# Kernel tuning notes

Measured on AMD Instinct MI355X. Metric: run time of the kernel, lower is better.

## Reference

```python
import jax, jax.numpy as jnp
import numpy as np

LOOPS = 2
NUM_GROUPS = 4
EXPERTS_PER_GROUP = 2
NUM_EXPERTS = NUM_GROUPS * EXPERTS_PER_GROUP
GROUPS_TOP_K = 2
TOP_K = 1
RMS_EPS = 1e-6
EPS = 1e-9


def setup_inputs() -> dict:
    key = jax.random.key(0)
    ks = jax.random.split(key, 6)
    B, S, D, F = 2, 1024, 1024, 2048
    return {
        "z": jax.random.normal(ks[0], (B, S, D), jnp.float32),
        "norm_w": jnp.ones((D,), jnp.float32),
        "w_macro": jax.random.normal(ks[1], (NUM_GROUPS, D), jnp.float32) * (D ** -0.5),
        "w_micro": jax.random.normal(ks[2], (NUM_GROUPS, EXPERTS_PER_GROUP, D), jnp.float32) * (D ** -0.5),
        "w1": jax.random.normal(ks[3], (NUM_EXPERTS, F, D), jnp.float32) * (D ** -0.5),
        "w2": jax.random.normal(ks[4], (NUM_EXPERTS, D, F), jnp.float32) * (F ** -0.5),
    }


def _rmsnorm(x, w):
    return x * jax.lax.rsqrt(jnp.mean(x * x, axis=-1, keepdims=True) + RMS_EPS) * w


def _combine_weights(x_flat, w_macro, w_micro):
    """Dense [T, E] combine matrix equivalent to the sort-based dispatch."""
    T = x_flat.shape[0]
    macro = jax.nn.softmax(x_flat @ w_macro.T, axis=-1)                    # [T, G]
    mvals, midx = jax.lax.top_k(macro, GROUPS_TOP_K)                       # [T, Gk]
    mvals = mvals / (jnp.sum(mvals, axis=-1, keepdims=True) + EPS)
    micro = jax.nn.softmax(jnp.einsum('td,ged->tge', x_flat, w_micro), axis=-1)  # [T, G, Eg]
    uvals, uidx = jax.lax.top_k(micro, TOP_K)                              # [T, G, k]
    uvals = uvals / (jnp.sum(uvals, axis=-1, keepdims=True) + EPS)
    tok = jnp.arange(T)
    combine = jnp.zeros((T, NUM_EXPERTS), x_flat.dtype)
    for s in range(GROUPS_TOP_K):
        g = midx[:, s]                                                     # [T]
        wg = mvals[:, s:s + 1]                                             # [T, 1]
        li = uidx[tok, g]                                                  # [T, k] local expert ids in group g
        lv = uvals[tok, g]                                                 # [T, k]
        eidx = g[:, None] * EXPERTS_PER_GROUP + li                         # [T, k] global expert ids
        combine = combine.at[tok[:, None], eidx].add(lv * wg)
    return combine


def reference(z, norm_w, w_macro, w_micro, w1, w2):
    B, S, D = z.shape
    T = B * S
    for _ in range(LOOPS):
        zn = _rmsnorm(z, norm_w)
        x = zn.reshape(T, D)
        combine = _combine_weights(x, w_macro, w_micro)                    # [T, E]
        # Dense equivalent of gather -> per-expert FFN -> weighted index_add
        h = jax.nn.silu(jnp.einsum('td,efd->tef', x, w1))                  # [T, E, F]
        y = jnp.einsum('tef,edf->ted', h, w2)                              # [T, E, D]
        mixed = jnp.einsum('ted,te->td', y, combine)                       # [T, D]
        z = z + mixed.reshape(B, S, D)
    return z
```

## Files before the change

### kernel.cpp

```cpp
#include <hip/hip_runtime.h>
#include <cstdint>
#include <cstddef>

#define T_TOK 2048
#define DDIM  1024
#define FDIM  2048

typedef __attribute__((ext_vector_type(8))) short bf16x8;
typedef __attribute__((ext_vector_type(4))) float f32x4;

static __device__ __forceinline__ float b2f(unsigned short u) {
  union { unsigned int i; float f; } v; v.i = ((unsigned int)u) << 16; return v.f;
}
static __device__ __forceinline__ unsigned short f2b(float f) {
  unsigned int x = __float_as_uint(f);
  return (unsigned short)((x + 0x7fffu + ((x >> 16) & 1u)) >> 16);
}
static __device__ __forceinline__ unsigned int pack2(float a, float b) {
  return (unsigned int)f2b(a) | ((unsigned int)f2b(b) << 16);
}

__global__ void k_probe(const unsigned int* __restrict__ nw, int* __restrict__ flag) {
  if (threadIdx.x == 0) flag[0] = (nw[0] == 0x3F800000u) ? 0 : 1;
}

__global__ void k_init(const void* __restrict__ zin, float* __restrict__ z32,
                       const int* __restrict__ flag) {
  const int i = blockIdx.x * blockDim.x + threadIdx.x;
  float4 f;
  if (flag[0]) {
    ushort4 u = ((const ushort4*)zin)[i];
    f.x = b2f(u.x); f.y = b2f(u.y); f.z = b2f(u.z); f.w = b2f(u.w);
  } else {
    f = ((const float4*)zin)[i];
  }
  ((float4*)z32)[i] = f;
}

__global__ void k_out(const float* __restrict__ z32, void* __restrict__ out,
                      const int* __restrict__ flag) {
  const int i = blockIdx.x * blockDim.x + threadIdx.x;
  const float4 a = ((const float4*)z32)[i];
  if (flag[0]) {
    ushort4 o; o.x = f2b(a.x); o.y = f2b(a.y); o.z = f2b(a.z); o.w = f2b(a.w);
    ((ushort4*)out)[i] = o;
  } else {
    ((float4*)out)[i] = a;
  }
}

__global__ void k_rms_route(const float* __restrict__ z32,
                            const void* __restrict__ nw,
                            const void* __restrict__ wmac,
                            const void* __restrict__ wmic,
                            const int* __restrict__ flag,
                            unsigned short* __restrict__ xh,
                            unsigned short* __restrict__ xl,
                            float* __restrict__ logits,
                            const int base)
{
  const int tl = blockIdx.x;
  const int t  = base + tl;
  const int tid = threadIdx.x;
  const int lane = tid & 63, wv = tid >> 6;
  const int isbf = flag[0];
  const float4 zv = ((const float4*)(z32 + (size_t)t * DDIM))[tid];
  float ss = zv.x*zv.x + zv.y*zv.y + zv.z*zv.z + zv.w*zv.w;
  #pragma unroll
  for (int o = 32; o > 0; o >>= 1) ss += __shfl_down(ss, o);
  __shared__ float red[4];
  __shared__ float lred[12][4];
  if (lane == 0) red[wv] = ss;
  __syncthreads();
  const float tot = red[0] + red[1] + red[2] + red[3];
  const float scale = 1.f / sqrtf(tot * (1.f / DDIM) + 1e-6f);
  float4 nwv;
  if (isbf) {
    ushort4 u = ((const ushort4*)nw)[tid];
    nwv.x = b2f(u.x); nwv.y = b2f(u.y); nwv.z = b2f(u.z); nwv.w = b2f(u.w);
  } else {
    nwv = ((const float4*)nw)[tid];
  }
  float4 xn;
  xn.x = zv.x * scale * nwv.x;
  xn.y = zv.y * scale * nwv.y;
  xn.z = zv.z * scale * nwv.z;
  xn.w = zv.w * scale * nwv.w;
  ushort4 h4, l4;
  h4.x = f2b(xn.x); l4.x = f2b(xn.x - b2f(h4.x));
  h4.y = f2b(xn.y); l4.y = f2b(xn.y - b2f(h4.y));
  h4.z = f2b(xn.z); l4.z = f2b(xn.z - b2f(h4.z));
  h4.w = f2b(xn.w); l4.w = f2b(xn.w - b2f(h4.w));
  ((ushort4*)(xh + (size_t)tl * DDIM))[tid] = h4;
  ((ushort4*)(xl + (size_t)tl * DDIM))[tid] = l4;

  float part[12];
  #pragma unroll
  for (int r = 0; r < 4; r++) {
    float4 w;
    if (isbf) {
      ushort4 u = ((const ushort4*)wmac)[r * 256 + tid];
      w.x = b2f(u.x); w.y = b2f(u.y); w.z = b2f(u.z); w.w = b2f(u.w);
    } else {
      w = ((const float4*)wmac)[r * 256 + tid];
    }
    part[r] = xn.x*w.x + xn.y*w.y + xn.z*w.z + xn.w*w.w;
  }
  #pragma unroll
  for (int r = 0; r < 8; r++) {
    float4 w;
    if (isbf) {
      ushort4 u = ((const ushort4*)wmic)[r * 256 + tid];
      w.x = b2f(u.x); w.y = b2f(u.y); w.z = b2f(u.z); w.w = b2f(u.w);
    } else {
      w = ((const float4*)wmic)[r * 256 + tid];
    }
    part[4 + r] = xn.x*w.x + xn.y*w.y + xn.z*w.z + xn.w*w.w;
  }
  #pragma unroll
  for (int r = 0; r < 12; r++) {
    float v = part[r];
    #pragma unroll
    for (int o = 32; o > 0; o >>= 1) v += __shfl_down(v, o);
    if (lane == 0) lred[r][wv] = v;
  }
  __syncthreads();
  if (tid < 12)
    logits[tl * 12 + tid] = lred[tid][0] + lred[tid][1] + lred[tid][2] + lred[tid][3];
}

__global__ void k_route_a(const float* __restrict__ logits, int* __restrict__ eidx,
                          float* __restrict__ cw, int* __restrict__ counts, const int Tc)
{
  const int t = blockIdx.x * 256 + threadIdx.x;
  if (t >= Tc) return;
  const float* lg = logits + t * 12;
  float p[4];
  float m = fmaxf(fmaxf(lg[0], lg[1]), fmaxf(lg[2], lg[3]));
  float s = 0.f;
  #pragma unroll
  for (int i = 0; i < 4; i++) { p[i] = expf(lg[i] - m); s += p[i]; }
  #pragma unroll
  for (int i = 0; i < 4; i++) p[i] /= s;
  int i1 = 0;
  #pragma unroll
  for (int i = 1; i < 4; i++) if (p[i] > p[i1]) i1 = i;
  int i2 = (i1 == 0) ? 1 : 0;
  #pragma unroll
  for (int i = 0; i < 4; i++) if (i != i1 && p[i] > p[i2]) i2 = i;
  const float denom = p[i1] + p[i2] + 1e-9f;
  const int gs[2] = { i1, i2 };
  #pragma unroll
  for (int sI = 0; sI < 2; sI++) {
    const int g = gs[sI];
    const float wg = p[g] / denom;
    const float u0 = lg[4 + 2*g], u1 = lg[4 + 2*g + 1];
    const int li = (u1 > u0) ? 1 : 0;
    const float uval = 1.f / (1.f + expf(-fabsf(u0 - u1)));
    const float lv = uval / (uval + 1e-9f);
    const int e = g * 2 + li;
    eidx[t*2 + sI] = e;
    cw[t*2 + sI] = wg * lv;
    atomicAdd(&counts[e], 1);
  }
}

__global__ void k_route_b(const int* __restrict__ counts, int* __restrict__ offsets) {
  if (threadIdx.x == 0) {
    int o = 0;
    for (int e = 0; e < 8; e++) { offsets[e] = o; o += counts[e]; }
    offsets[8] = o;
  }
}

__global__ void k_route_c(const int* __restrict__ eidx, const float* __restrict__ cw,
                          const int* __restrict__ offsets, int* __restrict__ counts2,
                          int* __restrict__ tok, float* __restrict__ wof, const int Tc)
{
  const int t = blockIdx.x * 256 + threadIdx.x;
  if (t >= Tc) return;
  #pragma unroll
  for (int sI = 0; sI < 2; sI++) {
    const int e = eidx[t*2 + sI];
    const int pos = atomicAdd(&counts2[e], 1);
    const int a = offsets[e] + pos;
    tok[a] = t;
    wof[a] = cw[t*2 + sI];
  }
}

template<int KDIM, bool IS_G1>
__launch_bounds__(256)
__global__ void k_gemm(const unsigned short* __restrict__ Ah,
                       const unsigned short* __restrict__ Al,
                       const void* __restrict__ Bw,
                       const int* __restrict__ flag,
                       const int* __restrict__ offsets,
                       const int* __restrict__ tok_of_a,
                       const float* __restrict__ w_of_a,
                       unsigned short* __restrict__ hh_out,
                       unsigned short* __restrict__ hl_out,
                       float* __restrict__ z32,
                       const int Nsize, const int base)
{
  const int e = blockIdx.z;
  const int offs = offsets[e];
  const int n_e = offsets[e + 1] - offs;
  const int rbase = blockIdx.y * 128;
  if (rbase >= n_e) return;
  const int cbase = blockIdx.x * 128;
  const int isbf = flag[0];

  __shared__ __align__(16) unsigned short Ahs[128 * 64];
  __shared__ __align__(16) unsigned short Als[128 * 64];
  __shared__ __align__(16) unsigned short Bhs[128 * 64];
  __shared__ __align__(16) unsigned short Bls[128 * 64];

  const int tid = threadIdx.x;
  const int lane = tid & 63;
  const int wv = tid >> 6;
  const int wr = (wv >> 1) * 64;
  const int wc = (wv & 1) * 64;
  const int lr = lane & 15;
  const int quad = lane >> 4;

  size_t aoff[4], boff[4];
  int loff[4];
  const int ch = tid & 7;
  const int gch = ch * 8;
  #pragma unroll
  for (int c = 0; c < 4; c++) {
    const int row = c * 32 + (tid >> 3);
    int rl = rbase + row; if (rl > n_e - 1) rl = n_e - 1;
    if constexpr (IS_G1) aoff[c] = (size_t)tok_of_a[offs + rl] * KDIM;
    else                 aoff[c] = (size_t)(offs + rl) * KDIM;
    boff[c] = ((size_t)e * Nsize + cbase + row) * (size_t)KDIM;
    loff[c] = row * 64 + ((ch ^ (row & 7)) * 8);
  }

  f32x4 acc[4][4];
  #pragma unroll
  for (int mt = 0; mt < 4; mt++)
    #pragma unroll
    for (int nt = 0; nt < 4; nt++)
      acc[mt][nt] = (f32x4){0.f, 0.f, 0.f, 0.f};

  for (int k0 = 0; k0 < KDIM; k0 += 64) {
    __syncthreads();
    #pragma unroll
    for (int c = 0; c < 4; c++) {
      *(uint4*)(&Ahs[loff[c]]) = *(const uint4*)(Ah + aoff[c] + k0 + gch);
      *(uint4*)(&Als[loff[c]]) = *(const uint4*)(Al + aoff[c] + k0 + gch);
    }
    if (isbf) {
      const unsigned short* B16 = (const unsigned short*)Bw;
      #pragma unroll
      for (int c = 0; c < 4; c++)
        *(uint4*)(&Bhs[loff[c]]) = *(const uint4*)(B16 + boff[c] + k0 + gch);
    } else {
      const float* B32 = (const float*)Bw;
      #pragma unroll
      for (int c = 0; c < 4; c++) {
        const float* bsrc = B32 + boff[c] + k0 + gch;
        const float4 v0 = *(const float4*)(bsrc);
        const float4 v1 = *(const float4*)(bsrc + 4);
        uint4 bh, bl;
        bh.x = pack2(v0.x, v0.y); bh.y = pack2(v0.z, v0.w);
        bh.z = pack2(v1.x, v1.y); bh.w = pack2(v1.z, v1.w);
        bl.x = pack2(v0.x - b2f((unsigned short)(bh.x & 0xFFFF)), v0.y - b2f((unsigned short)(bh.x >> 16)));
        bl.y = pack2(v0.z - b2f((unsigned short)(bh.y & 0xFFFF)), v0.w - b2f((unsigned short)(bh.y >> 16)));
        bl.z = pack2(v1.x - b2f((unsigned short)(bh.z & 0xFFFF)), v1.y - b2f((unsigned short)(bh.z >> 16)));
        bl.w = pack2(v1.z - b2f((unsigned short)(bh.w & 0xFFFF)), v1.w - b2f((unsigned short)(bh.w >> 16)));
        *(uint4*)(&Bhs[loff[c]]) = bh;
        *(uint4*)(&Bls[loff[c]]) = bl;
      }
    }
    __syncthreads();
    #pragma unroll
    for (int ks = 0; ks < 2; ks++) {
      const int swz = ((ks * 4 + quad) ^ (lr & 7)) * 8;
      bf16x8 af[4], alf[4], bhf[4];
      #pragma unroll
      for (int mt = 0; mt < 4; mt++) {
        const int r = wr + mt * 16 + lr;
        af[mt]  = *(const bf16x8*)(&Ahs[r * 64 + swz]);
        alf[mt] = *(const bf16x8*)(&Als[r * 64 + swz]);
      }
      #pragma unroll
      for (int nt = 0; nt < 4; nt++) {
        const int r = wc + nt * 16 + lr;
        bhf[nt] = *(const bf16x8*)(&Bhs[r * 64 + swz]);
      }
      if (isbf) {
        #pragma unroll
        for (int mt = 0; mt < 4; mt++)
          #pragma unroll
          for (int nt = 0; nt < 4; nt++) {
            acc[mt][nt] = __builtin_amdgcn_mfma_f32_16x16x32_bf16(af[mt],  bhf[nt], acc[mt][nt], 0, 0, 0);
            acc[mt][nt] = __builtin_amdgcn_mfma_f32_16x16x32_bf16(alf[mt], bhf[nt], acc[mt][nt], 0, 0, 0);
          }
      } else {
        bf16x8 blf[4];
        #pragma unroll
        for (int nt = 0; nt < 4; nt++) {
          const int r = wc + nt * 16 + lr;
          blf[nt] = *(const bf16x8*)(&Bls[r * 64 + swz]);
        }
        #pragma unroll
        for (int mt = 0; mt < 4; mt++)
          #pragma unroll
          for (int nt = 0; nt < 4; nt++) {
            acc[mt][nt] = __builtin_amdgcn_mfma_f32_16x16x32_bf16(af[mt],  bhf[nt], acc[mt][nt], 0, 0, 0);
            acc[mt][nt] = __builtin_amdgcn_mfma_f32_16x16x32_bf16(alf[mt], bhf[nt], acc[mt][nt], 0, 0, 0);
            acc[mt][nt] = __builtin_amdgcn_mfma_f32_16x16x32_bf16(af[mt],  blf[nt], acc[mt][nt], 0, 0, 0);
          }
      }
    }
  }

  #pragma unroll
  for (int mt = 0; mt < 4; mt++) {
    #pragma unroll
    for (int reg = 0; reg < 4; reg++) {
      const int rl = rbase + wr + mt * 16 + quad * 4 + reg;
      if (rl < n_e) {
        if constexpr (IS_G1) {
          const size_t ro = (size_t)(offs + rl) * Nsize;
          #pragma unroll
          for (int nt = 0; nt < 4; nt++) {
            const int col = cbase + wc + nt * 16 + lr;
            const float v = acc[mt][nt][reg];
            const float sv = v / (1.f + expf(-v));
            const unsigned short hi = f2b(sv);
            hh_out[ro + col] = hi;
            hl_out[ro + col] = f2b(sv - b2f(hi));
          }
        } else {
          const float w = w_of_a[offs + rl];
          const size_t to = (size_t)(base + tok_of_a[offs + rl]) * Nsize;
          #pragma unroll
          for (int nt = 0; nt < 4; nt++) {
            const int col = cbase + wc + nt * 16 + lr;
            atomicAdd(&z32[to + col], acc[mt][nt][reg] * w);
          }
        }
      }
    }
  }
}

extern "C" void kernel_launch(void* const* d_in, const int* in_sizes, int n_in,
                              void* d_out, int out_size, void* d_ws, size_t ws_size,
                              hipStream_t stream)
{
  (void)in_sizes; (void)n_in; (void)out_size;
  const void* z_in = d_in[0];
  const void* nw   = d_in[1];
  const void* wmac = d_in[2];
  const void* wmic = d_in[3];
  const void* w1   = d_in[4];
  const void* w2   = d_in[5];

  auto rup = [](size_t x) -> size_t { return (x + 255) & ~(size_t)255; };
  auto need = [&](int c) -> size_t {
    size_t Tc = T_TOK / c;
    size_t s = 0;
    s += rup(4);
    s += rup((size_t)T_TOK * DDIM * 4);
    s += rup(Tc * DDIM * 2) * 2;
    s += rup(Tc * 12 * 4);
    s += rup(Tc * 2 * 4) * 2;
    s += 256 + 256;
    s += rup(2 * Tc * 4) * 2;
    s += rup(2 * Tc * (size_t)FDIM * 2) * 2;
    return s;
  };
  int C = 8;
  if (need(1) <= ws_size) C = 1;
  else if (need(2) <= ws_size) C = 2;
  else if (need(4) <= ws_size) C = 4;
  const int Tc = T_TOK / C;

  char* ws = (char*)d_ws;
  size_t off = 0;
  auto alloc = [&](size_t bytes) -> void* {
    void* p = ws + off;
    off += rup(bytes);
    return p;
  };
  int* flag            = (int*)alloc(4);
  float* z32           = (float*)alloc((size_t)T_TOK * DDIM * 4);
  unsigned short* xh   = (unsigned short*)alloc((size_t)Tc * DDIM * 2);
  unsigned short* xl   = (unsigned short*)alloc((size_t)Tc * DDIM * 2);
  float* logits        = (float*)alloc((size_t)Tc * 12 * 4);
  int* eidx            = (int*)alloc((size_t)Tc * 2 * 4);
  float* cw            = (float*)alloc((size_t)Tc * 2 * 4);
  int* counts          = (int*)alloc(64);
  int* offsets         = (int*)alloc(64);
  int* tok             = (int*)alloc((size_t)2 * Tc * 4);
  float* wof           = (float*)alloc((size_t)2 * Tc * 4);
  unsigned short* hh   = (unsigned short*)alloc((size_t)2 * Tc * FDIM * 2);
  unsigned short* hl   = (unsigned short*)alloc((size_t)2 * Tc * FDIM * 2);

  k_probe<<<1, 64, 0, stream>>>((const unsigned int*)nw, flag);
  k_init<<<T_TOK * DDIM / 1024, 256, 0, stream>>>(z_in, z32, flag);
  for (int L = 0; L < 2; L++) {
    for (int cb = 0; cb < C; cb++) {
      const int base = cb * Tc;
      hipMemsetAsync(counts, 0, 64, stream);
      k_rms_route<<<Tc, 256, 0, stream>>>(z32, nw, wmac, wmic, flag, xh, xl, logits, base);
      k_route_a<<<Tc / 256, 256, 0, stream>>>(logits, eidx, cw, counts, Tc);
      k_route_b<<<1, 64, 0, stream>>>(counts, offsets);
      k_route_c<<<Tc / 256, 256, 0, stream>>>(eidx, cw, offsets, counts + 8, tok, wof, Tc);
      k_gemm<DDIM, true ><<<dim3(FDIM / 128, Tc / 128, 8), 256, 0, stream>>>(
          xh, xl, w1, flag, offsets, tok, nullptr, hh, hl, nullptr, FDIM, base);
      k_gemm<FDIM, false><<<dim3(DDIM / 128, Tc / 128, 8), 256, 0, stream>>>(
          hh, hl, w2, flag, offsets, tok, wof, nullptr, nullptr, z32, DDIM, base);
    }
  }
  k_out<<<T_TOK * DDIM / 1024, 256, 0, stream>>>(z32, d_out, flag);
}
```

Measured before the change: 709.7 us.

## Pre-split fp32 weights to bf16 hi/lo, direct-to-LDS loads, split-K second GEMM

When the workspace is large enough, the fp32 expert weights are split once per call into bf16 hi/lo arrays, so the GEMMs no longer convert them in every tile iteration. All tile loads now use global_load_lds to write straight into LDS while keeping the same swizzle. The second GEMM is split along K into two parts to launch more blocks, which relies on its epilogue accumulating into z32 atomically. The cost is a weight-conversion pass on every call and extra workspace memory.

```diff
diff --git a/kernel.cpp b/kernel.cpp
--- a/kernel.cpp
+++ b/kernel.cpp
@@ -18,6 +18,11 @@
 }
 static __device__ __forceinline__ unsigned int pack2(float a, float b) {
   return (unsigned int)f2b(a) | ((unsigned int)f2b(b) << 16);
+}
+static __device__ __forceinline__ void gload_lds16(const void* g, void* l) {
+  __builtin_amdgcn_global_load_lds(
+      (const __attribute__((address_space(1))) void*)g,
+      (__attribute__((address_space(3))) void*)l, 16, 0, 0);
 }
 
 __global__ void k_probe(const unsigned int* __restrict__ nw, int* __restrict__ flag) {
@@ -47,6 +52,20 @@
   } else {
     ((float4*)out)[i] = a;
   }
+}
+
+__global__ void k_split(const float* __restrict__ w, unsigned short* __restrict__ hi,
+                        unsigned short* __restrict__ lo, const int* __restrict__ flag) {
+  if (flag[0]) return;
+  const size_t i = (size_t)blockIdx.x * blockDim.x + threadIdx.x;
+  const float4 v = ((const float4*)w)[i];
+  ushort4 h, l;
+  h.x = f2b(v.x); l.x = f2b(v.x - b2f(h.x));
+  h.y = f2b(v.y); l.y = f2b(v.y - b2f(h.y));
+  h.z = f2b(v.z); l.z = f2b(v.z - b2f(h.z));
+  h.w = f2b(v.w); l.w = f2b(v.w - b2f(h.w));
+  ((ushort4*)hi)[i] = h;
+  ((ushort4*)lo)[i] = l;
 }
 
 __global__ void k_rms_route(const float* __restrict__ z32,
@@ -189,12 +208,15 @@
   }
 }
 
-template<int KDIM, bool IS_G1>
+template<int KDIM, bool IS_G1, int KSPLIT>
 __launch_bounds__(256)
 __global__ void k_gemm(const unsigned short* __restrict__ Ah,
                        const unsigned short* __restrict__ Al,
                        const void* __restrict__ Bw,
+                       const unsigned short* __restrict__ Bh_pre,
+                       const unsigned short* __restrict__ Bl_pre,
                        const int* __restrict__ flag,
+                       const int presplit,
                        const int* __restrict__ offsets,
                        const int* __restrict__ tok_of_a,
                        const float* __restrict__ w_of_a,
@@ -203,7 +225,8 @@
                        float* __restrict__ z32,
                        const int Nsize, const int base)
 {
-  const int e = blockIdx.z;
+  const int e = blockIdx.z / KSPLIT;
+  const int kpart = blockIdx.z - e * KSPLIT;
   const int offs = offsets[e];
   const int n_e = offsets[e + 1] - offs;
   const int rbase = blockIdx.y * 128;
@@ -225,9 +248,8 @@
   const int quad = lane >> 4;
 
   size_t aoff[4], boff[4];
-  int loff[4];
+  int gsw[4], loff[4];
   const int ch = tid & 7;
-  const int gch = ch * 8;
   #pragma unroll
   for (int c = 0; c < 4; c++) {
     const int row = c * 32 + (tid >> 3);
@@ -235,8 +257,12 @@
     if constexpr (IS_G1) aoff[c] = (size_t)tok_of_a[offs + rl] * KDIM;
     else                 aoff[c] = (size_t)(offs + rl) * KDIM;
     boff[c] = ((size_t)e * Nsize + cbase + row) * (size_t)KDIM;
-    loff[c] = row * 64 + ((ch ^ (row & 7)) * 8);
-  }
+    gsw[c]  = (ch ^ (row & 7)) * 8;
+    loff[c] = row * 64 + gsw[c];
+  }
+  int lbase[4];
+  #pragma unroll
+  for (int c = 0; c < 4; c++) lbase[c] = (c * 32 + wv * 8) * 64;
 
   f32x4 acc[4][4];
   #pragma unroll
@@ -245,23 +271,31 @@
     for (int nt = 0; nt < 4; nt++)
       acc[mt][nt] = (f32x4){0.f, 0.f, 0.f, 0.f};
 
-  for (int k0 = 0; k0 < KDIM; k0 += 64) {
+  const int KCH = KDIM / KSPLIT;
+  const int k_lo = kpart * KCH;
+  for (int k0 = k_lo; k0 < k_lo + KCH; k0 += 64) {
     __syncthreads();
     #pragma unroll
     for (int c = 0; c < 4; c++) {
-      *(uint4*)(&Ahs[loff[c]]) = *(const uint4*)(Ah + aoff[c] + k0 + gch);
-      *(uint4*)(&Als[loff[c]]) = *(const uint4*)(Al + aoff[c] + k0 + gch);
+      gload_lds16(Ah + aoff[c] + k0 + gsw[c], &Ahs[lbase[c]]);
+      gload_lds16(Al + aoff[c] + k0 + gsw[c], &Als[lbase[c]]);
     }
     if (isbf) {
       const unsigned short* B16 = (const unsigned short*)Bw;
       #pragma unroll
       for (int c = 0; c < 4; c++)
-        *(uint4*)(&Bhs[loff[c]]) = *(const uint4*)(B16 + boff[c] + k0 + gch);
+        gload_lds16(B16 + boff[c] + k0 + gsw[c], &Bhs[lbase[c]]);
+    } else if (presplit) {
+      #pragma unroll
+      for (int c = 0; c < 4; c++) {
+        gload_lds16(Bh_pre + boff[c] + k0 + gsw[c], &Bhs[lbase[c]]);
+        gload_lds16(Bl_pre + boff[c] + k0 + gsw[c], &Bls[lbase[c]]);
+      }
     } else {
       const float* B32 = (const float*)Bw;
       #pragma unroll
       for (int c = 0; c < 4; c++) {
-        const float* bsrc = B32 + boff[c] + k0 + gch;
+        const float* bsrc = B32 + boff[c] + k0 + (ch * 8);
         const float4 v0 = *(const float4*)(bsrc);
         const float4 v1 = *(const float4*)(bsrc + 4);
         uint4 bh, bl;
@@ -375,10 +409,16 @@
     s += rup(2 * Tc * (size_t)FDIM * 2) * 2;
     return s;
   };
-  int C = 8;
-  if (need(1) <= ws_size) C = 1;
+  const size_t WELEM = (size_t)8 * FDIM * DDIM;
+  const size_t wsplit_total = WELEM * 2 * 4;
+
+  int presplit = 0;
+  int C;
+  if (need(1) + wsplit_total <= ws_size) { C = 1; presplit = 1; }
+  else if (need(1) <= ws_size) C = 1;
   else if (need(2) <= ws_size) C = 2;
   else if (need(4) <= ws_size) C = 4;
+  else C = 8;
   const int Tc = T_TOK / C;
 
   char* ws = (char*)d_ws;
@@ -401,9 +441,21 @@
   float* wof           = (float*)alloc((size_t)2 * Tc * 4);
   unsigned short* hh   = (unsigned short*)alloc((size_t)2 * Tc * FDIM * 2);
   unsigned short* hl   = (unsigned short*)alloc((size_t)2 * Tc * FDIM * 2);
+  unsigned short *w1h = nullptr, *w1l = nullptr, *w2h = nullptr, *w2l = nullptr;
+  if (presplit) {
+    w1h = (unsigned short*)alloc(WELEM * 2);
+    w1l = (unsigned short*)alloc(WELEM * 2);
+    w2h = (unsigned short*)alloc(WELEM * 2);
+    w2l = (unsigned short*)alloc(WELEM * 2);
+  }
 
   k_probe<<<1, 64, 0, stream>>>((const unsigned int*)nw, flag);
   k_init<<<T_TOK * DDIM / 1024, 256, 0, stream>>>(z_in, z32, flag);
+  if (presplit) {
+    const int sb = (int)(WELEM / 4 / 256);
+    k_split<<<sb, 256, 0, stream>>>((const float*)w1, w1h, w1l, flag);
+    k_split<<<sb, 256, 0, stream>>>((const float*)w2, w2h, w2l, flag);
+  }
   for (int L = 0; L < 2; L++) {
     for (int cb = 0; cb < C; cb++) {
       const int base = cb * Tc;
@@ -412,10 +464,10 @@
       k_route_a<<<Tc / 256, 256, 0, stream>>>(logits, eidx, cw, counts, Tc);
       k_route_b<<<1, 64, 0, stream>>>(counts, offsets);
       k_route_c<<<Tc / 256, 256, 0, stream>>>(eidx, cw, offsets, counts + 8, tok, wof, Tc);
-      k_gemm<DDIM, true ><<<dim3(FDIM / 128, Tc / 128, 8), 256, 0, stream>>>(
-          xh, xl, w1, flag, offsets, tok, nullptr, hh, hl, nullptr, FDIM, base);
-      k_gemm<FDIM, false><<<dim3(DDIM / 128, Tc / 128, 8), 256, 0, stream>>>(
-          hh, hl, w2, flag, offsets, tok, wof, nullptr, nullptr, z32, DDIM, base);
+      k_gemm<DDIM, true, 1><<<dim3(FDIM / 128, Tc / 128, 8), 256, 0, stream>>>(
+          xh, xl, w1, w1h, w1l, flag, presplit, offsets, tok, nullptr, hh, hl, nullptr, FDIM, base);
+      k_gemm<FDIM, false, 2><<<dim3(DDIM / 128, Tc / 128, 16), 256, 0, stream>>>(
+          hh, hl, w2, w2h, w2l, flag, presplit, offsets, tok, wof, nullptr, nullptr, z32, DDIM, base);
     }
   }
   k_out<<<T_TOK * DDIM / 1024, 256, 0, stream>>>(z32, d_out, flag);
```

Result: faster. 613.2 us (-13.6%).
